# Performance work log

Hardware: AMD Instinct MI355X
Metric: run time of the kernel (lower is better)

The kernel has to match this reference:

```python
import jax, jax.numpy as jnp
import numpy as np

DIM = 128
HEADS = 8
RBF_K = 16
N_LIG = 20000
N_PROT = 80000
E = 262144
HEAD_DIM = DIM // HEADS
SCALE = HEAD_DIM ** -0.5


def setup_inputs() -> dict:
    key = jax.random.key(0)
    ks = jax.random.split(key, 16)
    inp = {
        "ligand_x": jax.random.normal(ks[0], (N_LIG, DIM), dtype=jnp.float32),
        "protein_x": jax.random.normal(ks[1], (N_PROT, DIM), dtype=jnp.float32),
        "cross_edges": jax.random.randint(ks[2], (E, 2), 0, N_LIG, dtype=jnp.int64)
        if jax.config.jax_enable_x64 else jax.random.randint(ks[2], (E, 2), 0, N_LIG, dtype=jnp.int32),
        "cross_attr": jax.random.uniform(ks[3], (E, RBF_K), dtype=jnp.float32),
        "Wq": jax.random.normal(ks[4], (DIM, DIM), dtype=jnp.float32) * (DIM ** -0.5),
        "bq": jax.random.normal(ks[5], (DIM,), dtype=jnp.float32) * 0.02,
        "Wk": jax.random.normal(ks[6], (DIM, DIM), dtype=jnp.float32) * (DIM ** -0.5),
        "bk": jax.random.normal(ks[7], (DIM,), dtype=jnp.float32) * 0.02,
        "Wv": jax.random.normal(ks[8], (DIM, DIM), dtype=jnp.float32) * (DIM ** -0.5),
        "bv": jax.random.normal(ks[9], (DIM,), dtype=jnp.float32) * 0.02,
        "Wo": jax.random.normal(ks[10], (DIM, DIM), dtype=jnp.float32) * (DIM ** -0.5),
        "bo": jax.random.normal(ks[11], (DIM,), dtype=jnp.float32) * 0.02,
        "Wr": jax.random.normal(ks[12], (RBF_K, HEADS), dtype=jnp.float32) * (RBF_K ** -0.5),
        "br": jax.random.normal(ks[13], (HEADS,), dtype=jnp.float32) * 0.02,
        "lig_start": 0,
        "prot_start": 0,
    }
    return inp


def _heads(t):
    return t.reshape(t.shape[0], HEADS, HEAD_DIM)


def _cross_attend(q_nodes, k_nodes, v_nodes, dst_idx, src_idx, rbf_bias, n_dst):
    # gather per-edge q/k/v: [E, H, D]
    qe = q_nodes[dst_idx]
    ke = k_nodes[src_idx]
    ve = v_nodes[src_idx]
    logits = jnp.einsum("ehd,ehd->eh", qe, ke) * SCALE + rbf_bias  # [E, H]
    # segment softmax over edges grouped by destination node
    m = jax.ops.segment_max(logits, dst_idx, num_segments=n_dst)  # [N, H]
    ex = jnp.exp(logits - m[dst_idx])
    s = jax.ops.segment_sum(ex, dst_idx, num_segments=n_dst)  # [N, H]
    w = ex / (s[dst_idx] + 1e-8)  # [E, H]
    agg = jax.ops.segment_sum(w[:, :, None] * ve, dst_idx, num_segments=n_dst)
    return agg.reshape(n_dst, HEADS * HEAD_DIM)


def reference(ligand_x, protein_x, cross_edges, cross_attr, Wq, bq, Wk, bk, Wv, bv,
              Wo, bo, Wr, br, lig_start, prot_start):
    n_lig, n_prot = ligand_x.shape[0], protein_x.shape[0]
    q_l = _heads(ligand_x @ Wq + bq)
    k_p = _heads(protein_x @ Wk + bk)
    v_p = _heads(protein_x @ Wv + bv)
    q_p = _heads(protein_x @ Wq + bq)
    k_l = _heads(ligand_x @ Wk + bk)
    v_l = _heads(ligand_x @ Wv + bv)

    lig_local = cross_edges[:, 0] - lig_start
    prot_local = cross_edges[:, 1] - prot_start
    rbf_bias = cross_attr @ Wr + br  # [E, heads]

    lig_agg = _cross_attend(q_l, k_p, v_p, lig_local, prot_local, rbf_bias, n_lig)
    prot_agg = _cross_attend(q_p, k_l, v_l, prot_local, lig_local, rbf_bias, n_prot)

    ligand_out = lig_agg @ Wo + bo   # dropout is identity at inference
    protein_out = prot_agg @ Wo + bo
    return (ligand_out, protein_out)
```

## Files before the change

kernel.cpp:

```cpp
#include <hip/hip_runtime.h>
#include <hip/hip_bf16.h>

typedef unsigned short u16;
typedef __attribute__((ext_vector_type(8))) short short8;
typedef __attribute__((ext_vector_type(4))) float f32x4;

__device__ __forceinline__ float bf2f(u16 u){
  union { unsigned int i; float f; } c; c.i = ((unsigned int)u) << 16; return c.f;
}
__device__ __forceinline__ u16 f2bf(float f){
  union { float f; unsigned int i; } c; c.f = f;
  unsigned int x = c.i;
  return (u16)((x + 0x7FFFu + ((x >> 16) & 1u)) >> 16);
}

__device__ __forceinline__ int edge_get(const int* __restrict__ e32, int i64, int e, int c){
  int idx = 2 * e + c;
  return i64 ? e32[2 * idx] : e32[idx];
}

__global__ void detect_kernel(const u16* __restrict__ lig16,
                              const int* __restrict__ e32, int* __restrict__ flags)
{
  int lane = threadIdx.x;
  int cnt = 0, nz = 0;
  #pragma unroll
  for (int j = 0; j < 4; j++){
    u16 u = lig16[(lane * 4 + j) * 2];
    int ex = (u >> 7) & 0xFF;
    if (ex >= 96 && ex < 160) cnt++;
    if (e32[(lane * 4 + j) * 2 + 1] != 0) nz++;
  }
  #pragma unroll
  for (int off = 1; off < 64; off <<= 1){
    cnt += __shfl_xor(cnt, off);
    nz  += __shfl_xor(nz, off);
  }
  if (lane == 0){
    flags[0] = (cnt < 128) ? 1 : 0;
    flags[1] = (nz == 0) ? 1 : 0;
  }
}

__global__ __launch_bounds__(256) void prep_w(
    const void* __restrict__ Wq, const void* __restrict__ Wk,
    const void* __restrict__ Wv, const void* __restrict__ Wo,
    const void* __restrict__ bq, const void* __restrict__ bk,
    const void* __restrict__ bv, const void* __restrict__ bo,
    u16* __restrict__ Wt, float* __restrict__ biasP, const int* __restrict__ flags)
{
  int mat = blockIdx.x, tid = threadIdx.x;
  const void* W = (mat == 0) ? Wq : (mat == 1) ? Wk : (mat == 2) ? Wv : Wo;
  const void* b = (mat == 0) ? bq : (mat == 1) ? bk : (mat == 2) ? bv : bo;
  int F = flags[0];
  u16* dst = Wt + mat * 16384;
  #pragma unroll 4
  for (int j = 0; j < 64; j++){
    int idx = tid + j * 256;
    u16 w = F ? f2bf(((const float*)W)[idx]) : ((const u16*)W)[idx];
    dst[(idx & 127) * 128 + (idx >> 7)] = w;
  }
  if (tid < 128)
    biasP[mat * 128 + tid] = F ? ((const float*)b)[tid] : bf2f(((const u16*)b)[tid]);
}

__global__ __launch_bounds__(256) void gemm_multi(
    const void* __restrict__ A0, int M0, const void* __restrict__ A1, int M1, int mb0,
    const u16* __restrict__ Wt, const float* __restrict__ biasP, int wbase, int nm,
    u16* __restrict__ O0b, u16* __restrict__ O1b, u16* __restrict__ O2b,
    float* __restrict__ O0f,
    int a_force_bf16, int final_out, const int* __restrict__ flags)
{
  __shared__ __align__(16) char smem[52224];
  u16 (*As)[136]  = (u16(*)[136])smem;
  u16 (*Ws)[136]  = (u16(*)[136])(smem + 17408);
  float (*Fs)[132] = (float(*)[132])(smem + 17408);

  int tid = threadIdx.x;
  int F = flags[0];
  int AF = a_force_bf16 ? 0 : F;
  int xb = blockIdx.x;
  const void* A; int M, m0, orow;
  if (xb < mb0){ A = A0; M = M0; m0 = xb * 64;          orow = m0; }
  else         { A = A1; M = M1; m0 = (xb - mb0) * 64;  orow = M0 + m0; }

  if (AF){
    const float* Af = (const float*)A;
    #pragma unroll
    for (int j = 0; j < 8; j++){
      int idx = tid + j * 256;
      int m = idx >> 5, k4 = idx & 31;
      float4 v = make_float4(0.f, 0.f, 0.f, 0.f);
      if (m0 + m < M) v = *(const float4*)&Af[(size_t)(m0 + m) * 128 + k4 * 4];
      ushort4 o; o.x = f2bf(v.x); o.y = f2bf(v.y); o.z = f2bf(v.z); o.w = f2bf(v.w);
      *(ushort4*)&As[m][k4 * 4] = o;
    }
  } else {
    const u16* Au = (const u16*)A;
    #pragma unroll
    for (int j = 0; j < 8; j++){
      int idx = tid + j * 256;
      int m = idx >> 5, k4 = idx & 31;
      ushort4 v = make_ushort4(0, 0, 0, 0);
      if (m0 + m < M) v = *(const ushort4*)&Au[(size_t)(m0 + m) * 128 + k4 * 4];
      *(ushort4*)&As[m][k4 * 4] = v;
    }
  }
  {
    const u16* Wsrc = Wt + (size_t)wbase * 16384;
    #pragma unroll
    for (int j = 0; j < 8; j++){
      int idx = tid + j * 256;
      *(short8*)&Ws[idx >> 4][(idx & 15) * 8] = *(const short8*)&Wsrc[idx * 8];
    }
  }
  __syncthreads();

  int wave = tid >> 6, lane = tid & 63;
  int quad = lane >> 4, ml = lane & 15;

  short8 af[4];
  #pragma unroll
  for (int kk = 0; kk < 4; kk++)
    af[kk] = *(const short8*)&As[wave * 16 + ml][kk * 32 + quad * 8];

  int f32out = final_out && F;

  for (int mat = 0; mat < nm; mat++){
    f32x4 acc[8];
    #pragma unroll
    for (int nt = 0; nt < 8; nt++) acc[nt] = (f32x4){0.f, 0.f, 0.f, 0.f};

    #pragma unroll
    for (int nt = 0; nt < 8; nt++){
      #pragma unroll
      for (int kk = 0; kk < 4; kk++){
        short8 bfr = *(const short8*)&Ws[nt * 16 + ml][kk * 32 + quad * 8];
        acc[nt] = __builtin_amdgcn_mfma_f32_16x16x32_bf16(af[kk], bfr, acc[nt], 0, 0, 0);
      }
    }

    __syncthreads();
    const float* bp = biasP + (size_t)(wbase + mat) * 128;
    #pragma unroll
    for (int nt = 0; nt < 8; nt++){
      float bcol = bp[nt * 16 + ml];
      #pragma unroll
      for (int r = 0; r < 4; r++)
        Fs[wave * 16 + quad * 4 + r][nt * 16 + ml] = acc[nt][r] + bcol;
    }
    __syncthreads();

    if (f32out){
      #pragma unroll
      for (int j = 0; j < 8; j++){
        int u = tid + j * 256;
        int row = u >> 5, c4 = (u & 31) * 4;
        if (m0 + row < M)
          *(float4*)&O0f[(size_t)(orow + row) * 128 + c4] = *(const float4*)&Fs[row][c4];
      }
    } else {
      u16* Cb = (mat == 0) ? O0b : ((mat == 1) ? O1b : O2b);
      #pragma unroll
      for (int j = 0; j < 4; j++){
        int u = tid + j * 256;
        int row = u >> 4, c8 = (u & 15) * 8;
        if (m0 + row < M){
          float4 x = *(const float4*)&Fs[row][c8];
          float4 y = *(const float4*)&Fs[row][c8 + 4];
          short8 s8;
          s8[0] = (short)f2bf(x.x); s8[1] = (short)f2bf(x.y);
          s8[2] = (short)f2bf(x.z); s8[3] = (short)f2bf(x.w);
          s8[4] = (short)f2bf(y.x); s8[5] = (short)f2bf(y.y);
          s8[6] = (short)f2bf(y.z); s8[7] = (short)f2bf(y.w);
          *(short8*)&Cb[(size_t)(orow + row) * 128 + c8] = s8;
        }
      }
    }

    if (mat + 1 < nm){
      __syncthreads();
      const u16* Wsrc = Wt + (size_t)(wbase + mat + 1) * 16384;
      #pragma unroll
      for (int j = 0; j < 8; j++){
        int idx = tid + j * 256;
        *(short8*)&Ws[idx >> 4][(idx & 15) * 8] = *(const short8*)&Wsrc[idx * 8];
      }
      __syncthreads();
    }
  }
}

__global__ __launch_bounds__(256) void edge_pre(
    const void* __restrict__ attr, const void* __restrict__ Wr,
    const void* __restrict__ br, float* __restrict__ ebias,
    const int* __restrict__ edges, const int* __restrict__ ls_p,
    const int* __restrict__ ps_p, int* __restrict__ cnt, int nlig, int E_,
    const int* __restrict__ flags)
{
  __shared__ float w[16][8];
  __shared__ float b[8];
  int tid = threadIdx.x;
  int F = flags[0];
  if (tid < 128) w[tid >> 3][tid & 7] = F ? ((const float*)Wr)[tid] : bf2f(((const u16*)Wr)[tid]);
  if (tid < 8)   b[tid] = F ? ((const float*)br)[tid] : bf2f(((const u16*)br)[tid]);
  __syncthreads();
  int e = blockIdx.x * 256 + tid;
  if (e >= E_) return;

  int I64 = flags[1];
  int dl = edge_get(edges, I64, e, 0) - ls_p[0];
  int dp = edge_get(edges, I64, e, 1) - ps_p[0];
  atomicAdd(&cnt[dl], 1);
  atomicAdd(&cnt[nlig + dp], 1);

  float a[16];
  if (F){
    const float* af = (const float*)attr;
    #pragma unroll
    for (int j = 0; j < 4; j++){
      float4 t = *(const float4*)&af[e * 16 + j * 4];
      a[4*j] = t.x; a[4*j+1] = t.y; a[4*j+2] = t.z; a[4*j+3] = t.w;
    }
  } else {
    const u16* au = (const u16*)attr;
    #pragma unroll
    for (int j = 0; j < 4; j++){
      ushort4 t = *(const ushort4*)&au[e * 16 + j * 4];
      a[4*j] = bf2f(t.x); a[4*j+1] = bf2f(t.y); a[4*j+2] = bf2f(t.z); a[4*j+3] = bf2f(t.w);
    }
  }
  #pragma unroll
  for (int hh = 0; hh < 8; hh++){
    float s = b[hh];
    #pragma unroll
    for (int r = 0; r < 16; r++) s += a[r] * w[r][hh];
    ebias[e * 8 + hh] = s;
  }
}

__global__ __launch_bounds__(256) void scan_blocksum(
    const int* __restrict__ cnt, int* __restrict__ bsum, int n)
{
  __shared__ int red[4];
  int tid = threadIdx.x;
  int i = blockIdx.x * 256 + tid;
  int v = (i < n) ? cnt[i] : 0;
  #pragma unroll
  for (int off = 1; off < 64; off <<= 1) v += __shfl_xor(v, off);
  if ((tid & 63) == 0) red[tid >> 6] = v;
  __syncthreads();
  if (tid == 0) bsum[blockIdx.x] = red[0] + red[1] + red[2] + red[3];
}

__global__ __launch_bounds__(512) void scan_bsum(
    int* __restrict__ bsum, int* __restrict__ boff, int nb)
{
  __shared__ int buf[512];
  int tid = threadIdx.x;
  int v = (tid < nb) ? bsum[tid] : 0;
  buf[tid] = v; __syncthreads();
  for (int off = 1; off < 512; off <<= 1){
    int t = (tid >= off) ? buf[tid - off] : 0;
    __syncthreads();
    buf[tid] += t;
    __syncthreads();
  }
  if (tid < nb) boff[tid] = buf[tid] - v;
}

__global__ __launch_bounds__(256) void scan_final(
    const int* __restrict__ cnt, const int* __restrict__ boff,
    int* __restrict__ offs, int* __restrict__ cursor, int n)
{
  __shared__ int buf[256];
  int tid = threadIdx.x;
  int i = blockIdx.x * 256 + tid;
  int v = (i < n) ? cnt[i] : 0;
  buf[tid] = v; __syncthreads();
  for (int off = 1; off < 256; off <<= 1){
    int t = (tid >= off) ? buf[tid - off] : 0;
    __syncthreads();
    buf[tid] += t;
    __syncthreads();
  }
  int excl = buf[tid] - v + boff[blockIdx.x];
  if (i < n){
    offs[i] = excl;
    cursor[i] = excl;
    if (i == n - 1) offs[n] = excl + v;
  }
}

__global__ __launch_bounds__(256) void scatter_kernel(
    const int* __restrict__ edges, const int* __restrict__ ls_p,
    const int* __restrict__ ps_p, int* __restrict__ cursor,
    int2* __restrict__ sorted, int nlig, int E_,
    const int* __restrict__ flags)
{
  int e = blockIdx.x * 256 + threadIdx.x;
  if (e >= E_) return;
  int I64 = flags[1];
  int dl = edge_get(edges, I64, e, 0) - ls_p[0];
  int dp = edge_get(edges, I64, e, 1) - ps_p[0];
  int p1 = atomicAdd(&cursor[dl], 1);        sorted[p1] = make_int2(e, nlig + dp);
  int p2 = atomicAdd(&cursor[nlig + dp], 1); sorted[p2] = make_int2(e, dl);
}

__global__ __launch_bounds__(256) void attn_kernel(
    const u16* __restrict__ Q, const u16* __restrict__ K, const u16* __restrict__ V,
    const int2* __restrict__ sorted, const int* __restrict__ offs,
    const float* __restrict__ ebias, u16* __restrict__ AGG, int ntot)
{
  int t = blockIdx.x * 4 + (threadIdx.x >> 6);
  if (t >= ntot) return;
  int lane = threadIdx.x & 63;
  int ql = lane & 15;
  int q4 = lane >> 4;
  int h  = ql >> 1;

  int beg = offs[t], end = offs[t + 1];

  if (beg == end){
    if (lane < 16){
      short8 z = {0, 0, 0, 0, 0, 0, 0, 0};
      *(short8*)&AGG[(size_t)t * 128 + ql * 8] = z;
    }
    return;
  }

  short8 qv = *(const short8*)&Q[(size_t)t * 128 + ql * 8];
  float qf[8];
  #pragma unroll
  for (int j = 0; j < 8; j++) qf[j] = bf2f((u16)qv[j]);

  float m = -1e30f, l = 0.f;
  float a[8];
  #pragma unroll
  for (int j = 0; j < 8; j++) a[j] = 0.f;

  int i = beg + q4;
  int2 cur = make_int2(0, 0), nxt = make_int2(0, 0);
  if (i < end)     cur = sorted[i];
  if (i + 4 < end) nxt = sorted[i + 4];

  short8 kA = {0,0,0,0,0,0,0,0}, vA = {0,0,0,0,0,0,0,0};
  float ebA = 0.f;
  if (i < end){
    kA = *(const short8*)&K[(size_t)cur.y * 128 + ql * 8];
    vA = *(const short8*)&V[(size_t)cur.y * 128 + ql * 8];
    ebA = ebias[(size_t)cur.x * 8 + h];
  }

  while (i < end){
    short8 kB = {0,0,0,0,0,0,0,0}, vB = {0,0,0,0,0,0,0,0};
    float ebB = 0.f;
    if (i + 4 < end){
      kB = *(const short8*)&K[(size_t)nxt.y * 128 + ql * 8];
      vB = *(const short8*)&V[(size_t)nxt.y * 128 + ql * 8];
      ebB = ebias[(size_t)nxt.x * 8 + h];
    }
    int2 n2 = make_int2(0, 0);
    if (i + 8 < end) n2 = sorted[i + 8];

    float s = 0.f;
    #pragma unroll
    for (int j = 0; j < 8; j++) s += qf[j] * bf2f((u16)kA[j]);
    s += __shfl_xor(s, 1);
    float logit = s * 0.25f + ebA;
    float nm = fmaxf(m, logit);
    float alpha = __expf(m - nm);
    float p = __expf(logit - nm);
    #pragma unroll
    for (int j = 0; j < 8; j++) a[j] = a[j] * alpha + p * bf2f((u16)vA[j]);
    l = l * alpha + p;
    m = nm;

    kA = kB; vA = vB; ebA = ebB;
    cur = nxt; nxt = n2;
    i += 4;
  }

  #pragma unroll
  for (int mask = 16; mask <= 32; mask <<= 1){
    float mo = __shfl_xor(m, mask);
    float lo = __shfl_xor(l, mask);
    float nm = fmaxf(m, mo);
    float sA = __expf(m - nm);
    float sB = __expf(mo - nm);
    l = l * sA + lo * sB;
    #pragma unroll
    for (int j = 0; j < 8; j++){
      float ao = __shfl_xor(a[j], mask);
      a[j] = a[j] * sA + ao * sB;
    }
    m = nm;
  }

  if (lane < 16){
    float inv = 1.f / (l + 1e-8f);
    short8 o;
    #pragma unroll
    for (int j = 0; j < 8; j++) o[j] = (short)f2bf(a[j] * inv);
    *(short8*)&AGG[(size_t)t * 128 + ql * 8] = o;
  }
}

extern "C" void kernel_launch(void* const* d_in, const int* in_sizes, int n_in,
                              void* d_out, int out_size, void* d_ws, size_t ws_size,
                              hipStream_t stream)
{
  const void* ligand_x  = d_in[0];
  const void* protein_x = d_in[1];
  const int* edges      = (const int*)d_in[2];
  const void* attr      = d_in[3];
  const void* Wq = d_in[4];  const void* bq = d_in[5];
  const void* Wk = d_in[6];  const void* bk = d_in[7];
  const void* Wv = d_in[8];  const void* bv = d_in[9];
  const void* Wo = d_in[10]; const void* bo = d_in[11];
  const void* Wr = d_in[12]; const void* br = d_in[13];
  const int* ls_p = (const int*)d_in[14];
  const int* ps_p = (const int*)d_in[15];

  const int nlig = in_sizes[0] / 128;
  const int nprot = in_sizes[1] / 128;
  const int E = in_sizes[2] / 2;
  const int ntot = nlig + nprot;

  char* w = (char*)d_ws;
  size_t off = 0;
  auto alloc = [&](size_t bytes) -> void* {
    void* p = w + off;
    off = (off + bytes + 255) & ~(size_t)255;
    return p;
  };
  int*   flags = (int*)alloc(256);
  u16*   Wt    = (u16*)alloc(4 * 16384 * 2);
  float* biasP = (float*)alloc(4 * 128 * 4);
  u16* Qb  = (u16*)alloc((size_t)ntot * 128 * 2);
  u16* Kb  = (u16*)alloc((size_t)ntot * 128 * 2);
  u16* Vb  = (u16*)alloc((size_t)ntot * 128 * 2);
  u16* AGG = (u16*)alloc((size_t)ntot * 128 * 2);
  float* ebias = (float*)alloc((size_t)E * 8 * 4);
  int* cnt    = (int*)alloc((size_t)ntot * 4);
  int* offs   = (int*)alloc((size_t)(ntot + 1) * 4);
  int* cursor = (int*)alloc((size_t)ntot * 4);
  int* bsum   = (int*)alloc(512 * 4);
  int* boff   = (int*)alloc(512 * 4);
  int2* sorted = (int2*)alloc((size_t)2 * E * 8);
  (void)ws_size; (void)n_in; (void)out_size;

  const int mb_l = (nlig + 63) / 64;
  const int mb_p = (nprot + 63) / 64;
  const int mb_t = (ntot + 63) / 64;
  const int eb = (E + 255) / 256;
  const int nb = (ntot + 255) / 256;

  hipMemsetAsync(cnt, 0, (size_t)ntot * 4, stream);
  detect_kernel<<<1, 64, 0, stream>>>((const u16*)ligand_x, edges, flags);
  prep_w<<<4, 256, 0, stream>>>(Wq, Wk, Wv, Wo, bq, bk, bv, bo, Wt, biasP, flags);

  gemm_multi<<<mb_l + mb_p, 256, 0, stream>>>(
      ligand_x, nlig, protein_x, nprot, mb_l,
      Wt, biasP, 0, 3,
      Qb, Kb, Vb, nullptr, 0, 0, flags);

  edge_pre<<<eb, 256, 0, stream>>>(attr, Wr, br, ebias, edges, ls_p, ps_p,
                                   cnt, nlig, E, flags);

  scan_blocksum<<<nb, 256, 0, stream>>>(cnt, bsum, ntot);
  scan_bsum<<<1, 512, 0, stream>>>(bsum, boff, nb);
  scan_final<<<nb, 256, 0, stream>>>(cnt, boff, offs, cursor, ntot);
  scatter_kernel<<<eb, 256, 0, stream>>>(edges, ls_p, ps_p, cursor, sorted, nlig, E, flags);

  attn_kernel<<<(ntot + 3) / 4, 256, 0, stream>>>(Qb, Kb, Vb, sorted, offs, ebias, AGG, ntot);

  gemm_multi<<<mb_t, 256, 0, stream>>>(
      AGG, ntot, nullptr, 0, mb_t,
      Wt, biasP, 3, 1,
      (u16*)d_out, nullptr, nullptr, (float*)d_out,
      1, 1, flags);
}
```

Baseline: 328.3 us.

## Make projection GEMM persistent with register prefetch and weights held in registers

The projection GEMM becomes a persistent grid-stride kernel capped at 1024 blocks. Each block prefetches the next 64-row A tile into registers while it computes the current one. Weight fragments now come straight from global memory into registers, each wave owning 32 output columns, instead of being staged through shared memory. The epilogue writes fp32 output directly and packs bf16 output in a smaller shared buffer, cutting LDS use so more blocks can be resident. In exchange, weight loads are repeated per tile through the cache, register pressure rises, and the fp32 direct stores are less coalesced.

After: 387.9 us. 18.2% more time.

```diff
diff --git a/kernel.cpp b/kernel.cpp
--- a/kernel.cpp
+++ b/kernel.cpp
@@ -64,130 +64,161 @@
     biasP[mat * 128 + tid] = F ? ((const float*)b)[tid] : bf2f(((const u16*)b)[tid]);
 }
 
-__global__ __launch_bounds__(256) void gemm_multi(
+__global__ __launch_bounds__(256, 4) void gemm_multi(
     const void* __restrict__ A0, int M0, const void* __restrict__ A1, int M1, int mb0,
     const u16* __restrict__ Wt, const float* __restrict__ biasP, int wbase, int nm,
     u16* __restrict__ O0b, u16* __restrict__ O1b, u16* __restrict__ O2b,
     float* __restrict__ O0f,
     int a_force_bf16, int final_out, const int* __restrict__ flags)
 {
-  __shared__ __align__(16) char smem[52224];
-  u16 (*As)[136]  = (u16(*)[136])smem;
-  u16 (*Ws)[136]  = (u16(*)[136])(smem + 17408);
-  float (*Fs)[132] = (float(*)[132])(smem + 17408);
+  __shared__ __align__(16) u16 As[64][136];
+  __shared__ __align__(16) u16 Fs[64][136];
 
   int tid = threadIdx.x;
   int F = flags[0];
   int AF = a_force_bf16 ? 0 : F;
-  int xb = blockIdx.x;
-  const void* A; int M, m0, orow;
-  if (xb < mb0){ A = A0; M = M0; m0 = xb * 64;          orow = m0; }
-  else         { A = A1; M = M1; m0 = (xb - mb0) * 64;  orow = M0 + m0; }
-
-  if (AF){
-    const float* Af = (const float*)A;
-    #pragma unroll
-    for (int j = 0; j < 8; j++){
-      int idx = tid + j * 256;
-      int m = idx >> 5, k4 = idx & 31;
-      float4 v = make_float4(0.f, 0.f, 0.f, 0.f);
-      if (m0 + m < M) v = *(const float4*)&Af[(size_t)(m0 + m) * 128 + k4 * 4];
-      ushort4 o; o.x = f2bf(v.x); o.y = f2bf(v.y); o.z = f2bf(v.z); o.w = f2bf(v.w);
-      *(ushort4*)&As[m][k4 * 4] = o;
-    }
-  } else {
-    const u16* Au = (const u16*)A;
-    #pragma unroll
-    for (int j = 0; j < 8; j++){
-      int idx = tid + j * 256;
-      int m = idx >> 5, k4 = idx & 31;
-      ushort4 v = make_ushort4(0, 0, 0, 0);
-      if (m0 + m < M) v = *(const ushort4*)&Au[(size_t)(m0 + m) * 128 + k4 * 4];
-      *(ushort4*)&As[m][k4 * 4] = v;
-    }
-  }
-  {
-    const u16* Wsrc = Wt + (size_t)wbase * 16384;
-    #pragma unroll
-    for (int j = 0; j < 8; j++){
-      int idx = tid + j * 256;
-      *(short8*)&Ws[idx >> 4][(idx & 15) * 8] = *(const short8*)&Wsrc[idx * 8];
-    }
-  }
-  __syncthreads();
-
+  int tiles1 = (M1 + 63) >> 6;
+  int TT = mb0 + tiles1;
   int wave = tid >> 6, lane = tid & 63;
   int quad = lane >> 4, ml = lane & 15;
-
-  short8 af[4];
-  #pragma unroll
-  for (int kk = 0; kk < 4; kk++)
-    af[kk] = *(const short8*)&As[wave * 16 + ml][kk * 32 + quad * 8];
-
   int f32out = final_out && F;
 
-  for (int mat = 0; mat < nm; mat++){
-    f32x4 acc[8];
-    #pragma unroll
-    for (int nt = 0; nt < 8; nt++) acc[nt] = (f32x4){0.f, 0.f, 0.f, 0.f};
-
-    #pragma unroll
-    for (int nt = 0; nt < 8; nt++){
+  float4 pf[8];
+
+  int tt0 = blockIdx.x;
+  if (tt0 < TT){
+    const void* A; int M, m0;
+    if (tt0 < mb0){ A = A0; M = M0; m0 = tt0 * 64; }
+    else          { A = A1; M = M1; m0 = (tt0 - mb0) * 64; }
+    if (AF){
+      const float* Af = (const float*)A;
+      #pragma unroll
+      for (int j = 0; j < 8; j++){
+        int u = tid + j * 256, row = u >> 5, c4 = (u & 31) * 4;
+        pf[j] = (m0 + row < M) ? *(const float4*)&Af[(size_t)(m0 + row) * 128 + c4]
+                               : make_float4(0.f, 0.f, 0.f, 0.f);
+      }
+    } else {
+      const float4* Au = (const float4*)A;
+      #pragma unroll
+      for (int j = 0; j < 4; j++){
+        int u = tid + j * 256, row = u >> 4, c8 = (u & 15);
+        pf[j] = (m0 + row < M) ? Au[(size_t)(m0 + row) * 16 + c8]
+                               : make_float4(0.f, 0.f, 0.f, 0.f);
+      }
+    }
+  }
+
+  for (int tt = blockIdx.x; tt < TT; tt += gridDim.x){
+    int M, m0, orow;
+    if (tt < mb0){ M = M0; m0 = tt * 64; orow = m0; }
+    else         { M = M1; m0 = (tt - mb0) * 64; orow = M0 + m0; }
+
+    if (AF){
+      #pragma unroll
+      for (int j = 0; j < 8; j++){
+        int u = tid + j * 256, row = u >> 5, c4 = (u & 31) * 4;
+        ushort4 o; o.x = f2bf(pf[j].x); o.y = f2bf(pf[j].y);
+        o.z = f2bf(pf[j].z); o.w = f2bf(pf[j].w);
+        *(ushort4*)&As[row][c4] = o;
+      }
+    } else {
+      #pragma unroll
+      for (int j = 0; j < 4; j++){
+        int u = tid + j * 256, row = u >> 4, c8 = (u & 15) * 8;
+        *(float4*)&As[row][c8] = pf[j];
+      }
+    }
+    __syncthreads();
+
+    int tn = tt + gridDim.x;
+    if (tn < TT){
+      const void* A; int Mn, m0n;
+      if (tn < mb0){ A = A0; Mn = M0; m0n = tn * 64; }
+      else         { A = A1; Mn = M1; m0n = (tn - mb0) * 64; }
+      if (AF){
+        const float* Af = (const float*)A;
+        #pragma unroll
+        for (int j = 0; j < 8; j++){
+          int u = tid + j * 256, row = u >> 5, c4 = (u & 31) * 4;
+          pf[j] = (m0n + row < Mn) ? *(const float4*)&Af[(size_t)(m0n + row) * 128 + c4]
+                                   : make_float4(0.f, 0.f, 0.f, 0.f);
+        }
+      } else {
+        const float4* Au = (const float4*)A;
+        #pragma unroll
+        for (int j = 0; j < 4; j++){
+          int u = tid + j * 256, row = u >> 4, c8 = (u & 15);
+          pf[j] = (m0n + row < Mn) ? Au[(size_t)(m0n + row) * 16 + c8]
+                                   : make_float4(0.f, 0.f, 0.f, 0.f);
+        }
+      }
+    }
+
+    for (int mat = 0; mat < nm; mat++){
+      const u16* wp = Wt + (size_t)(wbase + mat) * 16384
+                        + (size_t)(wave * 32 + ml) * 128 + quad * 8;
+      short8 wf0[4], wf1[4];
       #pragma unroll
       for (int kk = 0; kk < 4; kk++){
-        short8 bfr = *(const short8*)&Ws[nt * 16 + ml][kk * 32 + quad * 8];
-        acc[nt] = __builtin_amdgcn_mfma_f32_16x16x32_bf16(af[kk], bfr, acc[nt], 0, 0, 0);
-      }
-    }
-
+        wf0[kk] = *(const short8*)&wp[kk * 32];
+        wf1[kk] = *(const short8*)&wp[2048 + kk * 32];
+      }
+      float b0 = biasP[(wbase + mat) * 128 + wave * 32 + ml];
+      float b1 = biasP[(wbase + mat) * 128 + wave * 32 + 16 + ml];
+
+      f32x4 acc[4][2];
+      #pragma unroll
+      for (int mt = 0; mt < 4; mt++){
+        acc[mt][0] = (f32x4){0.f, 0.f, 0.f, 0.f};
+        acc[mt][1] = (f32x4){0.f, 0.f, 0.f, 0.f};
+      }
+
+      #pragma unroll
+      for (int mt = 0; mt < 4; mt++){
+        #pragma unroll
+        for (int kk = 0; kk < 4; kk++){
+          short8 af = *(const short8*)&As[mt * 16 + ml][kk * 32 + quad * 8];
+          acc[mt][0] = __builtin_amdgcn_mfma_f32_16x16x32_bf16(af, wf0[kk], acc[mt][0], 0, 0, 0);
+          acc[mt][1] = __builtin_amdgcn_mfma_f32_16x16x32_bf16(af, wf1[kk], acc[mt][1], 0, 0, 0);
+        }
+      }
+
+      if (f32out){
+        #pragma unroll
+        for (int mt = 0; mt < 4; mt++){
+          #pragma unroll
+          for (int r = 0; r < 4; r++){
+            int row = mt * 16 + quad * 4 + r;
+            if (m0 + row < M){
+              float* op = &O0f[(size_t)(orow + row) * 128 + wave * 32 + ml];
+              op[0]  = acc[mt][0][r] + b0;
+              op[16] = acc[mt][1][r] + b1;
+            }
+          }
+        }
+      } else {
+        if (mat > 0) __syncthreads();
+        #pragma unroll
+        for (int mt = 0; mt < 4; mt++){
+          #pragma unroll
+          for (int r = 0; r < 4; r++){
+            int row = mt * 16 + quad * 4 + r;
+            Fs[row][wave * 32 + ml]      = f2bf(acc[mt][0][r] + b0);
+            Fs[row][wave * 32 + 16 + ml] = f2bf(acc[mt][1][r] + b1);
+          }
+        }
+        __syncthreads();
+        u16* Cb = (mat == 0) ? O0b : ((mat == 1) ? O1b : O2b);
+        #pragma unroll
+        for (int j = 0; j < 4; j++){
+          int u = tid + j * 256, row = u >> 4, c8 = (u & 15) * 8;
+          if (m0 + row < M)
+            *(short8*)&Cb[(size_t)(orow + row) * 128 + c8] = *(const short8*)&Fs[row][c8];
+        }
+      }
+    }
     __syncthreads();
-    const float* bp = biasP + (size_t)(wbase + mat) * 128;
-    #pragma unroll
-    for (int nt = 0; nt < 8; nt++){
-      float bcol = bp[nt * 16 + ml];
-      #pragma unroll
-      for (int r = 0; r < 4; r++)
-        Fs[wave * 16 + quad * 4 + r][nt * 16 + ml] = acc[nt][r] + bcol;
-    }
-    __syncthreads();
-
-    if (f32out){
-      #pragma unroll
-      for (int j = 0; j < 8; j++){
-        int u = tid + j * 256;
-        int row = u >> 5, c4 = (u & 31) * 4;
-        if (m0 + row < M)
-          *(float4*)&O0f[(size_t)(orow + row) * 128 + c4] = *(const float4*)&Fs[row][c4];
-      }
-    } else {
-      u16* Cb = (mat == 0) ? O0b : ((mat == 1) ? O1b : O2b);
-      #pragma unroll
-      for (int j = 0; j < 4; j++){
-        int u = tid + j * 256;
-        int row = u >> 4, c8 = (u & 15) * 8;
-        if (m0 + row < M){
-          float4 x = *(const float4*)&Fs[row][c8];
-          float4 y = *(const float4*)&Fs[row][c8 + 4];
-          short8 s8;
-          s8[0] = (short)f2bf(x.x); s8[1] = (short)f2bf(x.y);
-          s8[2] = (short)f2bf(x.z); s8[3] = (short)f2bf(x.w);
-          s8[4] = (short)f2bf(y.x); s8[5] = (short)f2bf(y.y);
-          s8[6] = (short)f2bf(y.z); s8[7] = (short)f2bf(y.w);
-          *(short8*)&Cb[(size_t)(orow + row) * 128 + c8] = s8;
-        }
-      }
-    }
-
-    if (mat + 1 < nm){
-      __syncthreads();
-      const u16* Wsrc = Wt + (size_t)(wbase + mat + 1) * 16384;
-      #pragma unroll
-      for (int j = 0; j < 8; j++){
-        int idx = tid + j * 256;
-        *(short8*)&Ws[idx >> 4][(idx & 15) * 8] = *(const short8*)&Wsrc[idx * 8];
-      }
-      __syncthreads();
-    }
   }
 }
 
@@ -460,7 +491,10 @@
   detect_kernel<<<1, 64, 0, stream>>>((const u16*)ligand_x, edges, flags);
   prep_w<<<4, 256, 0, stream>>>(Wq, Wk, Wv, Wo, bq, bk, bv, bo, Wt, biasP, flags);
 
-  gemm_multi<<<mb_l + mb_p, 256, 0, stream>>>(
+  const int TT1 = mb_l + mb_p;
+  int g1 = TT1 < 1024 ? TT1 : 1024;
+  if (g1 < 1) g1 = 1;
+  gemm_multi<<<g1, 256, 0, stream>>>(
       ligand_x, nlig, protein_x, nprot, mb_l,
       Wt, biasP, 0, 3,
       Qb, Kb, Vb, nullptr, 0, 0, flags);
@@ -475,7 +509,9 @@
 
   attn_kernel<<<(ntot + 3) / 4, 256, 0, stream>>>(Qb, Kb, Vb, sorted, offs, ebias, AGG, ntot);
 
-  gemm_multi<<<mb_t, 256, 0, stream>>>(
+  int g2 = mb_t < 1024 ? mb_t : 1024;
+  if (g2 < 1) g2 = 1;
+  gemm_multi<<<g2, 256, 0, stream>>>(
       AGG, ntot, nullptr, 0, mb_t,
       Wt, biasP, 3, 1,
       (u16*)d_out, nullptr, nullptr, (float*)d_out,
```
